# Kernel tuning notes

Hardware: AMD Instinct MI355X
Metric: run time of the kernel (lower is better)

The kernel has to match this reference:

```python
import jax, jax.numpy as jnp
import numpy as np

LN_EPS = 1e-5
TOP_K = 2

def _layernorm(x, g, b):
    mu = jnp.mean(x, axis=-1, keepdims=True)
    var = jnp.mean(jnp.square(x - mu), axis=-1, keepdims=True)
    return (x - mu) * jax.lax.rsqrt(var + LN_EPS) * g + b

def setup_inputs() -> dict:
    key = jax.random.key(0)
    ks = jax.random.split(key, 8)
    N, D, H, E = 16384, 2048, 256, 64
    H2 = H // 2
    s = 0.02
    return {
        "x": jax.random.normal(ks[0], (N, D), dtype=jnp.float32),
        "w1": jax.random.normal(ks[1], (D, H), dtype=jnp.float32) * s,
        "b1": jnp.zeros((H,), jnp.float32),
        "g1": jnp.ones((H,), jnp.float32),
        "be1": jnp.zeros((H,), jnp.float32),
        "w2": jax.random.normal(ks[2], (H, H2), dtype=jnp.float32) * s,
        "b2": jnp.zeros((H2,), jnp.float32),
        "g2": jnp.ones((H2,), jnp.float32),
        "be2": jnp.zeros((H2,), jnp.float32),
        "w3": jax.random.normal(ks[3], (H2, E), dtype=jnp.float32) * s,
        "b3": jnp.zeros((E,), jnp.float32),
        "temperature": jnp.ones((1,), jnp.float32),
    }

def reference(x, w1, b1, g1, be1, w2, b2, g2, be2, w3, b3, temperature):
    # Router MLP: Linear -> LN -> GELU (exact/erf, matching torch F.gelu) x2
    h = jax.nn.gelu(_layernorm(x @ w1 + b1, g1, be1), approximate=False)
    h = jax.nn.gelu(_layernorm(h @ w2 + b2, g2, be2), approximate=False)
    gate_logits = h @ w3 + b3  # [N, E]
    gate_logits = gate_logits / jnp.maximum(temperature, 0.1)
    # eval mode: dropout off, no noise injection
    top_vals, top_idx = jax.lax.top_k(gate_logits, TOP_K)  # [N, k]
    top_gates = jax.nn.softmax(top_vals, axis=-1)
    top_gates = top_gates / (jnp.sum(top_gates, axis=-1, keepdims=True) + 1e-8)
    rows = jnp.arange(gate_logits.shape[0])[:, None]
    gates = jnp.zeros_like(gate_logits).at[rows, top_idx].set(top_gates)
    return gates, top_idx, gate_logits
```

## Files before the change

kernel.cpp:

```cpp
#include <hip/hip_runtime.h>
#include <math.h>

#define NROWS 16384
#define DIN   2048
#define H1D   256
#define H2D   128
#define NE    64
#define EPS_MARGIN 2e-4f
#define SQRT1_2 0.70710678118654752440084436210485
#define IBIG 0x7fffffff

typedef short  bf16x8 __attribute__((ext_vector_type(8)));
typedef float  f32x4  __attribute__((ext_vector_type(4)));
typedef __attribute__((address_space(3))) void lds_void;
typedef __attribute__((address_space(1))) const void glob_void;

#define GLDS16(src, dst) \
    __builtin_amdgcn_global_load_lds((glob_void*)(src), (lds_void*)(dst), 16, 0, 0)

#define WS_OFF_ROWS 64
#define WS_OFF_W1FH 66560
#define WS_OFF_W1FL (WS_OFF_W1FH + DIN*H1D*2)
#define WS_OFF_H1G  (WS_OFF_W1FL + DIN*H1D*2)
#define WS_NEED_FUSED (size_t)WS_OFF_H1G
#define WS_NEED_SPLIT (size_t)(WS_OFF_H1G + (size_t)NROWS*H1D*4)

__device__ __forceinline__ void split_bf16(float v, unsigned short& h, unsigned short& l) {
    unsigned int u = __float_as_uint(v);
    unsigned int rh = u + 0x7FFFu + ((u >> 16) & 1u);
    h = (unsigned short)(rh >> 16);
    float hf = __uint_as_float((unsigned int)h << 16);
    float r = v - hf;
    unsigned int u2 = __float_as_uint(r);
    unsigned int rl = u2 + 0x7FFFu + ((u2 >> 16) & 1u);
    l = (unsigned short)(rl >> 16);
}

__device__ __forceinline__ void split_fast(float v, short& h, short& l) {
    unsigned int u = __float_as_uint(v);
    unsigned int rh = (u + 0x7FFFu + ((u >> 16) & 1u)) >> 16;
    h = (short)rh;
    float r = v - __uint_as_float(rh << 16);
    l = (short)(__float_as_uint(r) >> 16);
}

__device__ __forceinline__ bool gtr(float a, int ia, float b, int ib) {
    return a > b || (a == b && ia < ib);
}
__device__ __forceinline__ void ins3(float v, int iv,
                                     float& t1, int& j1, float& t2, int& j2, float& t3, int& j3) {
    if (gtr(v, iv, t1, j1))      { t3 = t2; j3 = j2; t2 = t1; j2 = j1; t1 = v; j1 = iv; }
    else if (gtr(v, iv, t2, j2)) { t3 = t2; j3 = j2; t2 = v;  j2 = iv; }
    else if (gtr(v, iv, t3, j3)) { t3 = v;  j3 = iv; }
}

__global__ void prep_w1f_kernel(const float* __restrict__ w1,
                                unsigned short* __restrict__ w1f_hi,
                                unsigned short* __restrict__ w1f_lo,
                                unsigned int* __restrict__ ws_count)
{
    if (blockIdx.x == 0 && threadIdx.x == 0) *ws_count = 0u;
    const int g    = blockIdx.x * 256 + threadIdx.x;
    const int st   = g >> 10;
    const int cb   = (g >> 6) & 15;
    const int lane = g & 63;
    const int col  = cb * 16 + (lane & 15);
    const int k0   = st * 32 + (lane >> 4) * 8;
    unsigned short vh[8], vl[8];
    #pragma unroll
    for (int j = 0; j < 8; ++j) {
        float v = w1[(size_t)(k0 + j) * H1D + col];
        split_bf16(v, vh[j], vl[j]);
    }
    *(uint4*)(w1f_hi + (size_t)g * 8) = *(uint4*)vh;
    *(uint4*)(w1f_lo + (size_t)g * 8) = *(uint4*)vl;
}

#define BM 32
#define KSTEPS (DIN / 32)
#define OFF_AB  0
#define OFF_BH  8192
#define OFF_BL  40960
#define OFF_H1  0
#define H1P     264
#define OFF_H2  33792
#define H2P     132
#define OFF_RED 50688
#define SMEM_SZ 73728

__global__ __launch_bounds__(512, 4)
void gemm1_ln_kernel(const float* __restrict__ x,
                     const float* __restrict__ b1, const float* __restrict__ g1,
                     const float* __restrict__ be1,
                     const unsigned short* __restrict__ w1f_hi,
                     const unsigned short* __restrict__ w1f_lo,
                     float* __restrict__ h1g)
{
    __shared__ __align__(16) char smem[SMEM_SZ];
    float*  sH1  = (float*)(smem + OFF_H1);
    float2* sRed = (float2*)(smem + OFF_RED);

    const int tid  = threadIdx.x;
    const int lane = tid & 63;
    const int wid  = tid >> 6;
    const int wr   = wid >> 2;
    const int wc   = wid & 3;
    const int lr   = lane & 15;
    const int lg   = lane >> 4;
    const int r0   = blockIdx.x * BM;

    const int arow = (wid & 3) * 8 + (lane >> 3);
    const int aseg = lane & 7;
    const float* asrc = x + (size_t)(r0 + arow) * DIN + ((aseg ^ (arow & 7)) << 2);
    const unsigned short* bsh0 = w1f_hi + ((size_t)((wid * 2 + 0) * 64 + lane)) * 8;
    const unsigned short* bsh1 = w1f_hi + ((size_t)((wid * 2 + 1) * 64 + lane)) * 8;
    const unsigned short* bsl0 = w1f_lo + ((size_t)((wid * 2 + 0) * 64 + lane)) * 8;
    const unsigned short* bsl1 = w1f_lo + ((size_t)((wid * 2 + 1) * 64 + lane)) * 8;

#define STAGE(buf_, st_) do { \
    if (wid < 4) GLDS16(asrc + (size_t)(st_) * 32, smem + OFF_AB + (buf_) * 4096 + wid * 1024); \
    GLDS16(bsh0 + (size_t)(st_) * 8192, smem + OFF_BH + (buf_) * 16384 + (wid * 2 + 0) * 1024); \
    GLDS16(bsh1 + (size_t)(st_) * 8192, smem + OFF_BH + (buf_) * 16384 + (wid * 2 + 1) * 1024); \
    GLDS16(bsl0 + (size_t)(st_) * 8192, smem + OFF_BL + (buf_) * 16384 + (wid * 2 + 0) * 1024); \
    GLDS16(bsl1 + (size_t)(st_) * 8192, smem + OFF_BL + (buf_) * 16384 + (wid * 2 + 1) * 1024); \
} while (0)

    f32x4 acc[4];
    #pragma unroll
    for (int t = 0; t < 4; ++t) acc[t] = (f32x4){0.f, 0.f, 0.f, 0.f};

    STAGE(0, 0);
    __syncthreads();
    int cur = 0;
    for (int st = 0; st < KSTEPS; ++st) {
        if (st + 1 < KSTEPS) STAGE(cur ^ 1, st + 1);
        bf16x8 ah, al;
        {
            int row = wr * 16 + lr;
            int g0  = (2 * lg) ^ (lr & 7);
            const char* abase = smem + OFF_AB + cur * 4096 + row * 128;
            float4 q0 = *(const float4*)(abase + g0 * 16);
            float4 q1 = *(const float4*)(abase + (g0 ^ 1) * 16);
            float af[8] = {q0.x, q0.y, q0.z, q0.w, q1.x, q1.y, q1.z, q1.w};
            #pragma unroll
            for (int j = 0; j < 8; ++j) {
                short h, l;
                split_fast(af[j], h, l);
                ah[j] = h; al[j] = l;
            }
        }
        bf16x8 bh[4], bl[4];
        #pragma unroll
        for (int t = 0; t < 4; ++t) {
            int cb = wc * 4 + t;
            bh[t] = *(const bf16x8*)(smem + OFF_BH + cur * 16384 + cb * 1024 + lane * 16);
            bl[t] = *(const bf16x8*)(smem + OFF_BL + cur * 16384 + cb * 1024 + lane * 16);
        }
        #pragma unroll
        for (int t = 0; t < 4; ++t) {
            acc[t] = __builtin_amdgcn_mfma_f32_16x16x32_bf16(ah, bh[t], acc[t], 0, 0, 0);
            acc[t] = __builtin_amdgcn_mfma_f32_16x16x32_bf16(ah, bl[t], acc[t], 0, 0, 0);
            acc[t] = __builtin_amdgcn_mfma_f32_16x16x32_bf16(al, bh[t], acc[t], 0, 0, 0);
        }
        __syncthreads();
        cur ^= 1;
    }
#undef STAGE

    float tb[4], tg[4], tbe[4];
    #pragma unroll
    for (int t = 0; t < 4; ++t) {
        int col = wc * 64 + t * 16 + lr;
        tb[t] = b1[col]; tg[t] = g1[col]; tbe[t] = be1[col];
    }
    #pragma unroll
    for (int t = 0; t < 4; ++t)
        #pragma unroll
        for (int rg = 0; rg < 4; ++rg)
            acc[t][rg] += tb[t];

    #pragma unroll
    for (int rg = 0; rg < 4; ++rg) {
        float p1 = 0.f, p2 = 0.f;
        #pragma unroll
        for (int t = 0; t < 4; ++t) { float v = acc[t][rg]; p1 += v; p2 += v * v; }
        p1 += __shfl_xor(p1, 1, 64); p2 += __shfl_xor(p2, 1, 64);
        p1 += __shfl_xor(p1, 2, 64); p2 += __shfl_xor(p2, 2, 64);
        p1 += __shfl_xor(p1, 4, 64); p2 += __shfl_xor(p2, 4, 64);
        p1 += __shfl_xor(p1, 8, 64); p2 += __shfl_xor(p2, 8, 64);
        if (lr == 0) {
            int row = wr * 16 + lg * 4 + rg;
            sRed[row * 4 + wc] = make_float2(p1, p2);
        }
    }
    __syncthreads();

    #pragma unroll
    for (int rg = 0; rg < 4; ++rg) {
        int row = wr * 16 + lg * 4 + rg;
        float2 q0 = sRed[row * 4 + 0], q1 = sRed[row * 4 + 1];
        float2 q2 = sRed[row * 4 + 2], q3 = sRed[row * 4 + 3];
        float s1 = (q0.x + q1.x) + (q2.x + q3.x);
        float s2 = (q0.y + q1.y) + (q2.y + q3.y);
        float mu  = s1 * (1.0f / H1D);
        float var = s2 * (1.0f / H1D) - mu * mu;
        float rs  = rsqrtf(var + 1e-5f);
        #pragma unroll
        for (int t = 0; t < 4; ++t) {
            int col = wc * 64 + t * 16 + lr;
            float v = (acc[t][rg] - mu) * rs * tg[t] + tbe[t];
            v = 0.5f * v * (1.0f + erff(v * (float)SQRT1_2));
            sH1[row * H1P + col] = v;
        }
    }
    __syncthreads();

    #pragma unroll
    for (int i = 0; i < 4; ++i) {
        int u = tid + i * 512;
        int row = u >> 6, f4 = u & 63;
        float4 v = *(const float4*)&sH1[row * H1P + f4 * 4];
        *(float4*)(h1g + (size_t)(r0 + row) * H1D + f4 * 4) = v;
    }
}

__global__ __launch_bounds__(256, 4)
void tail_kernel(const float* __restrict__ h1g,
                 const float* __restrict__ w2, const float* __restrict__ b2,
                 const float* __restrict__ g2, const float* __restrict__ be2,
                 const float* __restrict__ w3, const float* __restrict__ b3,
                 const float* __restrict__ temperature,
                 float* __restrict__ out_gates,
                 float* __restrict__ out_idx,
                 float* __restrict__ out_logits,
                 unsigned int* __restrict__ ws_count,
                 int* __restrict__ ws_rows)
{
    __shared__ __align__(16) float sH1[16 * H1P];
    __shared__ __align__(16) float sH2[16 * H2P];

    const int tid = threadIdx.x;
    const int r0  = blockIdx.x * 16;

    #pragma unroll
    for (int i = 0; i < 4; ++i) {
        int u = tid + i * 256;
        int row = u >> 6, f4 = u & 63;
        *(float4*)&sH1[row * H1P + f4 * 4] =
            *(const float4*)(h1g + (size_t)(r0 + row) * H1D + f4 * 4);
    }
    __syncthreads();

    const int tx = tid & 31;
    const int ty = tid >> 5;
    float acc2[2][4];
    #pragma unroll
    for (int i = 0; i < 2; ++i)
        #pragma unroll
        for (int j = 0; j < 4; ++j) acc2[i][j] = 0.f;
    {
        const float* w2p = w2 + tx * 4;
        #pragma unroll 4
        for (int k = 0; k < H1D; ++k) {
            float4 wv4 = *(const float4*)(w2p + (size_t)k * H2D);
            float wr4[4] = {wv4.x, wv4.y, wv4.z, wv4.w};
            float ar0 = sH1[(ty * 2 + 0) * H1P + k];
            float ar1 = sH1[(ty * 2 + 1) * H1P + k];
            #pragma unroll
            for (int j = 0; j < 4; ++j) {
                acc2[0][j] = fmaf(ar0, wr4[j], acc2[0][j]);
                acc2[1][j] = fmaf(ar1, wr4[j], acc2[1][j]);
            }
        }
    }
    {
        float b2v[4], g2v[4], be2v[4];
        #pragma unroll
        for (int j = 0; j < 4; ++j) {
            b2v[j] = b2[tx * 4 + j]; g2v[j] = g2[tx * 4 + j]; be2v[j] = be2[tx * 4 + j];
        }
        #pragma unroll
        for (int i = 0; i < 2; ++i) {
            float s1 = 0.f, s2 = 0.f, vv[4];
            #pragma unroll
            for (int j = 0; j < 4; ++j) {
                float v = acc2[i][j] + b2v[j];
                vv[j] = v; s1 += v; s2 += v * v;
            }
            s1 += __shfl_xor(s1, 1, 64);  s2 += __shfl_xor(s2, 1, 64);
            s1 += __shfl_xor(s1, 2, 64);  s2 += __shfl_xor(s2, 2, 64);
            s1 += __shfl_xor(s1, 4, 64);  s2 += __shfl_xor(s2, 4, 64);
            s1 += __shfl_xor(s1, 8, 64);  s2 += __shfl_xor(s2, 8, 64);
            s1 += __shfl_xor(s1, 16, 64); s2 += __shfl_xor(s2, 16, 64);
            float mu  = s1 * (1.0f / H2D);
            float var = s2 * (1.0f / H2D) - mu * mu;
            float rs  = rsqrtf(var + 1e-5f);
            #pragma unroll
            for (int j = 0; j < 4; ++j) {
                float v = (vv[j] - mu) * rs * g2v[j] + be2v[j];
                v = 0.5f * v * (1.0f + erff(v * (float)SQRT1_2));
                sH2[(ty * 2 + i) * H2P + tx * 4 + j] = v;
            }
        }
    }
    __syncthreads();

    const int q = tid & 15;
    const int r = tid >> 4;
    float acc3[4];
    #pragma unroll
    for (int j = 0; j < 4; ++j) acc3[j] = 0.f;
    {
        const float* w3p = w3 + q * 4;
        #pragma unroll 4
        for (int k = 0; k < H2D; ++k) {
            float hv = sH2[r * H2P + k];
            float4 wa = *(const float4*)(w3p + (size_t)k * NE);
            acc3[0] = fmaf(hv, wa.x, acc3[0]);
            acc3[1] = fmaf(hv, wa.y, acc3[1]);
            acc3[2] = fmaf(hv, wa.z, acc3[2]);
            acc3[3] = fmaf(hv, wa.w, acc3[3]);
        }
    }
    float tinv = 1.0f / fmaxf(temperature[0], 0.1f);
    float lg4[4];
    #pragma unroll
    for (int j = 0; j < 4; ++j) lg4[j] = (acc3[j] + b3[q * 4 + j]) * tinv;

    *(float4*)(out_logits + (size_t)(r0 + r) * NE + q * 4) = make_float4(lg4[0], lg4[1], lg4[2], lg4[3]);

    float v1 = -INFINITY, v2 = -INFINITY, v3 = -INFINITY;
    int   i1 = IBIG, i2 = IBIG, i3 = IBIG;
    #pragma unroll
    for (int j = 0; j < 4; ++j) ins3(lg4[j], q * 4 + j, v1, i1, v2, i2, v3, i3);
    #pragma unroll
    for (int m = 1; m < 16; m <<= 1) {
        float c1v = __shfl_xor(v1, m, 64); int cj1 = __shfl_xor(i1, m, 64);
        float c2v = __shfl_xor(v2, m, 64); int cj2 = __shfl_xor(i2, m, 64);
        float c3v = __shfl_xor(v3, m, 64); int cj3 = __shfl_xor(i3, m, 64);
        ins3(c1v, cj1, v1, i1, v2, i2, v3, i3);
        ins3(c2v, cj2, v1, i1, v2, i2, v3, i3);
        ins3(c3v, cj3, v1, i1, v2, i2, v3, i3);
    }

    float e2  = expf(v2 - v1);
    float den = 1.0f + e2;
    float tg1 = 1.0f / den;
    float tg2 = e2 / den;
    float ssum = tg1 + tg2 + 1e-8f;
    float gv1 = tg1 / ssum;
    float gv2 = tg2 / ssum;

    if (q == 0) {
        float margin = fminf(v1 - v2, v2 - v3);
        if (!(margin >= EPS_MARGIN)) {
            unsigned int slot = atomicAdd(ws_count, 1u);
            if ((int)slot < NROWS) ws_rows[slot] = r0 + r;
        }
        out_idx[(size_t)(r0 + r) * 2 + 0] = (float)i1;
        out_idx[(size_t)(r0 + r) * 2 + 1] = (float)i2;
    }
    {
        float gvv[4];
        #pragma unroll
        for (int j = 0; j < 4; ++j) {
            int c = q * 4 + j;
            gvv[j] = (c == i1) ? gv1 : ((c == i2) ? gv2 : 0.0f);
        }
        *(float4*)(out_gates + (size_t)(r0 + r) * NE + q * 4) = make_float4(gvv[0], gvv[1], gvv[2], gvv[3]);
    }
}

__global__ __launch_bounds__(1024, 1)
void repair_f64_kernel(const float* __restrict__ x,
                       const float* __restrict__ w1, const float* __restrict__ b1,
                       const float* __restrict__ g1, const float* __restrict__ be1,
                       const float* __restrict__ w2, const float* __restrict__ b2,
                       const float* __restrict__ g2, const float* __restrict__ be2,
                       const float* __restrict__ w3, const float* __restrict__ b3,
                       const float* __restrict__ temperature,
                       float* __restrict__ out_gates,
                       float* __restrict__ out_idx,
                       const unsigned int* __restrict__ ws_count,
                       const int* __restrict__ ws_rows)
{
    __shared__ float  sxr[DIN];
    __shared__ double sPart[1024];
    __shared__ double sh1[H1D];
    __shared__ double sh2[H2D];
    __shared__ double sred[32];

    const int t = threadIdx.x;
    const int lane = t & 63, w = t >> 6;
    const unsigned int n = *ws_count;
    const double tinv = 1.0 / fmax((double)temperature[0], 0.1);

    for (unsigned int wi = blockIdx.x; wi < n; wi += gridDim.x) {
        const int row = ws_rows[wi];

        const float4* xr4 = (const float4*)(x + (size_t)row * DIN);
        if (t < DIN / 4) ((float4*)sxr)[t] = xr4[t];
        __syncthreads();

        {
            const int c = t & 255, sl = t >> 8;
            const float* w1c = w1 + c;
            const int kb = sl * 512;
            double a0 = 0, a1 = 0, a2 = 0, a3 = 0;
            for (int k = 0; k < 512; k += 16) {
                float wv[16];
                #pragma unroll
                for (int j = 0; j < 16; ++j)
                    wv[j] = w1c[(size_t)(kb + k + j) * H1D];
                float xv[16];
                #pragma unroll
                for (int j = 0; j < 16; ++j) xv[j] = sxr[kb + k + j];
                #pragma unroll
                for (int j = 0; j < 16; j += 4) {
                    a0 = fma((double)xv[j + 0], (double)wv[j + 0], a0);
                    a1 = fma((double)xv[j + 1], (double)wv[j + 1], a1);
                    a2 = fma((double)xv[j + 2], (double)wv[j + 2], a2);
                    a3 = fma((double)xv[j + 3], (double)wv[j + 3], a3);
                }
            }
            sPart[sl * 256 + c] = (a0 + a1) + (a2 + a3);
        }
        __syncthreads();
        double c1 = 0.0;
        if (t < 256) {
            c1 = ((sPart[0 * 256 + t] + sPart[1 * 256 + t]) +
                  (sPart[2 * 256 + t] + sPart[3 * 256 + t])) + (double)b1[t];
            double s1 = c1, s2 = c1 * c1;
            for (int m = 1; m < 64; m <<= 1) { s1 += __shfl_xor(s1, m, 64); s2 += __shfl_xor(s2, m, 64); }
            if (lane == 0) { sred[w * 2] = s1; sred[w * 2 + 1] = s2; }
        }
        __syncthreads();
        if (t < 256) {
            double s1 = (sred[0] + sred[2]) + (sred[4] + sred[6]);
            double s2 = (sred[1] + sred[3]) + (sred[5] + sred[7]);
            double mu  = s1 * (1.0 / H1D);
            double var = s2 * (1.0 / H1D) - mu * mu;
            double rs  = 1.0 / sqrt(var + 1e-5);
            double vn  = (c1 - mu) * rs * (double)g1[t] + (double)be1[t];
            sh1[t] = 0.5 * vn * (1.0 + erf(vn * SQRT1_2));
        }
        __syncthreads();

        {
            const int c = t & 127, sl2 = t >> 7;
            const float* w2c = w2 + c;
            const int kb = sl2 * 32;
            float w2v[32];
            #pragma unroll
            for (int j = 0; j < 32; ++j)
                w2v[j] = w2c[(size_t)(kb + j) * H2D];
            double p = 0;
            #pragma unroll
            for (int j = 0; j < 32; ++j)
                p = fma(sh1[kb + j], (double)w2v[j], p);
            sPart[sl2 * 128 + c] = p;
        }
        __syncthreads();
        double c2 = 0.0;
        if (t < 128) {
            double p0 = (sPart[0 * 128 + t] + sPart[1 * 128 + t]) + (sPart[2 * 128 + t] + sPart[3 * 128 + t]);
            double p1 = (sPart[4 * 128 + t] + sPart[5 * 128 + t]) + (sPart[6 * 128 + t] + sPart[7 * 128 + t]);
            c2 = (p0 + p1) + (double)b2[t];
            double s1 = c2, s2 = c2 * c2;
            for (int m = 1; m < 64; m <<= 1) { s1 += __shfl_xor(s1, m, 64); s2 += __shfl_xor(s2, m, 64); }
            if (lane == 0) { sred[w * 2] = s1; sred[w * 2 + 1] = s2; }
        }
        __syncthreads();
        if (t < 128) {
            double s1 = sred[0] + sred[2];
            double s2 = sred[1] + sred[3];
            double mu  = s1 * (1.0 / H2D);
            double var = s2 * (1.0 / H2D) - mu * mu;
            double rs  = 1.0 / sqrt(var + 1e-5);
            double vn  = (c2 - mu) * rs * (double)g2[t] + (double)be2[t];
            sh2[t] = 0.5 * vn * (1.0 + erf(vn * SQRT1_2));
        }
        __syncthreads();

        {
            const int c = t & 63, sl3 = t >> 6;
            const float* w3c = w3 + c;
            const int kb = sl3 * 8;
            float w3v[8];
            #pragma unroll
            for (int j = 0; j < 8; ++j)
                w3v[j] = w3c[(size_t)(kb + j) * NE];
            double p = 0;
            #pragma unroll
            for (int j = 0; j < 8; ++j)
                p = fma(sh2[kb + j], (double)w3v[j], p);
            sPart[sl3 * 64 + c] = p;
        }
        __syncthreads();
        if (t < NE) {
            double q0 = (sPart[0*64+t]  + sPart[1*64+t])  + (sPart[2*64+t]  + sPart[3*64+t]);
            double q1 = (sPart[4*64+t]  + sPart[5*64+t])  + (sPart[6*64+t]  + sPart[7*64+t]);
            double q2 = (sPart[8*64+t]  + sPart[9*64+t])  + (sPart[10*64+t] + sPart[11*64+t]);
            double q3 = (sPart[12*64+t] + sPart[13*64+t]) + (sPart[14*64+t] + sPart[15*64+t]);
            double lgv = (((q0 + q1) + (q2 + q3)) + (double)b3[t]) * tinv;

            double v1 = lgv, v2 = -INFINITY;
            int i1 = t, i2 = IBIG;
            for (int m = 1; m < 64; m <<= 1) {
                double ov1 = __shfl_xor(v1, m, 64); int oi1 = __shfl_xor(i1, m, 64);
                double ov2 = __shfl_xor(v2, m, 64); int oi2 = __shfl_xor(i2, m, 64);
                bool aw = (v1 > ov1) || (v1 == ov1 && i1 < oi1);
                double wv = aw ? v1  : ov1;  int wi_ = aw ? i1  : oi1;
                double lv = aw ? ov1 : v1;   int li  = aw ? oi1 : i1;
                double sv = aw ? v2  : ov2;  int si  = aw ? i2  : oi2;
                bool sw = (sv > lv) || (sv == lv && si < li);
                v1 = wv; i1 = wi_;
                v2 = sw ? sv : lv;
                i2 = sw ? si : li;
            }
            double e2d = exp(v2 - v1);
            double den = 1.0 + e2d;
            double tg1 = 1.0 / den;
            double tg2 = e2d / den;
            double ssum = tg1 + tg2 + 1e-8;
            float gv1 = (float)(tg1 / ssum);
            float gv2 = (float)(tg2 / ssum);
            if (t == 0) {
                out_idx[(size_t)row * 2 + 0] = (float)i1;
                out_idx[(size_t)row * 2 + 1] = (float)i2;
            }
            out_gates[(size_t)row * NE + t] = (t == i1) ? gv1 : ((t == i2) ? gv2 : 0.0f);
        }
        __syncthreads();
    }
}

__global__ __launch_bounds__(512, 4)
void gate_fused_kernel(const float* __restrict__ x,
                       const float* __restrict__ b1, const float* __restrict__ g1,
                       const float* __restrict__ be1,
                       const float* __restrict__ w2, const float* __restrict__ b2,
                       const float* __restrict__ g2, const float* __restrict__ be2,
                       const float* __restrict__ w3, const float* __restrict__ b3,
                       const float* __restrict__ temperature,
                       const unsigned short* __restrict__ w1f_hi,
                       const unsigned short* __restrict__ w1f_lo,
                       float* __restrict__ out_gates,
                       float* __restrict__ out_idx,
                       float* __restrict__ out_logits,
                       unsigned int* __restrict__ ws_count,
                       int* __restrict__ ws_rows)
{
    __shared__ __align__(16) char smem[SMEM_SZ];
    float*  sH1  = (float*)(smem + OFF_H1);
    float*  sH2  = (float*)(smem + OFF_H2);
    float2* sRed = (float2*)(smem + OFF_RED);

    const int tid  = threadIdx.x;
    const int lane = tid & 63;
    const int wid  = tid >> 6;
    const int wr   = wid >> 2;
    const int wc   = wid & 3;
    const int lr   = lane & 15;
    const int lg   = lane >> 4;
    const int r0   = blockIdx.x * BM;

    const int arow = (wid & 3) * 8 + (lane >> 3);
    const int aseg = lane & 7;
    const float* asrc = x + (size_t)(r0 + arow) * DIN + ((aseg ^ (arow & 7)) << 2);
    const unsigned short* bsh0 = w1f_hi + ((size_t)((wid * 2 + 0) * 64 + lane)) * 8;
    const unsigned short* bsh1 = w1f_hi + ((size_t)((wid * 2 + 1) * 64 + lane)) * 8;
    const unsigned short* bsl0 = w1f_lo + ((size_t)((wid * 2 + 0) * 64 + lane)) * 8;
    const unsigned short* bsl1 = w1f_lo + ((size_t)((wid * 2 + 1) * 64 + lane)) * 8;

#define STAGE(buf_, st_) do { \
    if (wid < 4) GLDS16(asrc + (size_t)(st_) * 32, smem + OFF_AB + (buf_) * 4096 + wid * 1024); \
    GLDS16(bsh0 + (size_t)(st_) * 8192, smem + OFF_BH + (buf_) * 16384 + (wid * 2 + 0) * 1024); \
    GLDS16(bsh1 + (size_t)(st_) * 8192, smem + OFF_BH + (buf_) * 16384 + (wid * 2 + 1) * 1024); \
    GLDS16(bsl0 + (size_t)(st_) * 8192, smem + OFF_BL + (buf_) * 16384 + (wid * 2 + 0) * 1024); \
    GLDS16(bsl1 + (size_t)(st_) * 8192, smem + OFF_BL + (buf_) * 16384 + (wid * 2 + 1) * 1024); \
} while (0)

    f32x4 acc[4];
    #pragma unroll
    for (int t = 0; t < 4; ++t) acc[t] = (f32x4){0.f, 0.f, 0.f, 0.f};

    STAGE(0, 0);
    __syncthreads();
    int cur = 0;
    for (int st = 0; st < KSTEPS; ++st) {
        if (st + 1 < KSTEPS) STAGE(cur ^ 1, st + 1);
        bf16x8 ah, al;
        {
            int row = wr * 16 + lr;
            int g0  = (2 * lg) ^ (lr & 7);
            const char* abase = smem + OFF_AB + cur * 4096 + row * 128;
            float4 q0 = *(const float4*)(abase + g0 * 16);
            float4 q1 = *(const float4*)(abase + (g0 ^ 1) * 16);
            float af[8] = {q0.x, q0.y, q0.z, q0.w, q1.x, q1.y, q1.z, q1.w};
            #pragma unroll
            for (int j = 0; j < 8; ++j) {
                short h, l;
                split_fast(af[j], h, l);
                ah[j] = h; al[j] = l;
            }
        }
        bf16x8 bh[4], bl[4];
        #pragma unroll
        for (int t = 0; t < 4; ++t) {
            int cb = wc * 4 + t;
            bh[t] = *(const bf16x8*)(smem + OFF_BH + cur * 16384 + cb * 1024 + lane * 16);
            bl[t] = *(const bf16x8*)(smem + OFF_BL + cur * 16384 + cb * 1024 + lane * 16);
        }
        #pragma unroll
        for (int t = 0; t < 4; ++t) {
            acc[t] = __builtin_amdgcn_mfma_f32_16x16x32_bf16(ah, bh[t], acc[t], 0, 0, 0);
            acc[t] = __builtin_amdgcn_mfma_f32_16x16x32_bf16(ah, bl[t], acc[t], 0, 0, 0);
            acc[t] = __builtin_amdgcn_mfma_f32_16x16x32_bf16(al, bh[t], acc[t], 0, 0, 0);
        }
        __syncthreads();
        cur ^= 1;
    }
#undef STAGE

    float tb[4], tg[4], tbe[4];
    #pragma unroll
    for (int t = 0; t < 4; ++t) {
        int col = wc * 64 + t * 16 + lr;
        tb[t] = b1[col]; tg[t] = g1[col]; tbe[t] = be1[col];
    }
    #pragma unroll
    for (int t = 0; t < 4; ++t)
        #pragma unroll
        for (int rg = 0; rg < 4; ++rg)
            acc[t][rg] += tb[t];

    #pragma unroll
    for (int rg = 0; rg < 4; ++rg) {
        float p1 = 0.f, p2 = 0.f;
        #pragma unroll
        for (int t = 0; t < 4; ++t) { float v = acc[t][rg]; p1 += v; p2 += v * v; }
        p1 += __shfl_xor(p1, 1, 64); p2 += __shfl_xor(p2, 1, 64);
        p1 += __shfl_xor(p1, 2, 64); p2 += __shfl_xor(p2, 2, 64);
        p1 += __shfl_xor(p1, 4, 64); p2 += __shfl_xor(p2, 4, 64);
        p1 += __shfl_xor(p1, 8, 64); p2 += __shfl_xor(p2, 8, 64);
        if (lr == 0) {
            int row = wr * 16 + lg * 4 + rg;
            sRed[row * 4 + wc] = make_float2(p1, p2);
        }
    }
    __syncthreads();

    #pragma unroll
    for (int rg = 0; rg < 4; ++rg) {
        int row = wr * 16 + lg * 4 + rg;
        float2 q0 = sRed[row * 4 + 0], q1 = sRed[row * 4 + 1];
        float2 q2 = sRed[row * 4 + 2], q3 = sRed[row * 4 + 3];
        float s1 = (q0.x + q1.x) + (q2.x + q3.x);
        float s2 = (q0.y + q1.y) + (q2.y + q3.y);
        float mu  = s1 * (1.0f / H1D);
        float var = s2 * (1.0f / H1D) - mu * mu;
        float rs  = rsqrtf(var + 1e-5f);
        #pragma unroll
        for (int t = 0; t < 4; ++t) {
            int col = wc * 64 + t * 16 + lr;
            float v = (acc[t][rg] - mu) * rs * tg[t] + tbe[t];
            v = 0.5f * v * (1.0f + erff(v * (float)SQRT1_2));
            sH1[row * H1P + col] = v;
        }
    }
    __syncthreads();

    const int tx = tid & 31;
    const int ty = tid >> 5;
    float acc2[2][4];
    #pragma unroll
    for (int i = 0; i < 2; ++i)
        #pragma unroll
        for (int j = 0; j < 4; ++j) acc2[i][j] = 0.f;
    {
        const float* w2p = w2 + tx * 4;
        #pragma unroll 4
        for (int k = 0; k < H1D; ++k) {
            float4 wv4 = *(const float4*)(w2p + (size_t)k * H2D);
            float wr4[4] = {wv4.x, wv4.y, wv4.z, wv4.w};
            float ar0 = sH1[(ty * 2 + 0) * H1P + k];
            float ar1 = sH1[(ty * 2 + 1) * H1P + k];
            #pragma unroll
            for (int j = 0; j < 4; ++j) {
                acc2[0][j] = fmaf(ar0, wr4[j], acc2[0][j]);
                acc2[1][j] = fmaf(ar1, wr4[j], acc2[1][j]);
            }
        }
    }
    {
        float b2v[4], g2v[4], be2v[4];
        #pragma unroll
        for (int j = 0; j < 4; ++j) {
            b2v[j] = b2[tx * 4 + j]; g2v[j] = g2[tx * 4 + j]; be2v[j] = be2[tx * 4 + j];
        }
        #pragma unroll
        for (int i = 0; i < 2; ++i) {
            float s1 = 0.f, s2 = 0.f, vv[4];
            #pragma unroll
            for (int j = 0; j < 4; ++j) {
                float v = acc2[i][j] + b2v[j];
                vv[j] = v; s1 += v; s2 += v * v;
            }
            s1 += __shfl_xor(s1, 1, 64);  s2 += __shfl_xor(s2, 1, 64);
            s1 += __shfl_xor(s1, 2, 64);  s2 += __shfl_xor(s2, 2, 64);
            s1 += __shfl_xor(s1, 4, 64);  s2 += __shfl_xor(s2, 4, 64);
            s1 += __shfl_xor(s1, 8, 64);  s2 += __shfl_xor(s2, 8, 64);
            s1 += __shfl_xor(s1, 16, 64); s2 += __shfl_xor(s2, 16, 64);
            float mu  = s1 * (1.0f / H2D);
            float var = s2 * (1.0f / H2D) - mu * mu;
            float rs  = rsqrtf(var + 1e-5f);
            #pragma unroll
            for (int j = 0; j < 4; ++j) {
                float v = (vv[j] - mu) * rs * g2v[j] + be2v[j];
                v = 0.5f * v * (1.0f + erff(v * (float)SQRT1_2));
                sH2[(ty * 2 + i) * H2P + tx * 4 + j] = v;
            }
        }
    }
    __syncthreads();

    const int q = tid & 15;
    const int r = tid >> 4;
    float acc3[4];
    #pragma unroll
    for (int j = 0; j < 4; ++j) acc3[j] = 0.f;
    {
        const float* w3p = w3 + q * 4;
        #pragma unroll 4
        for (int k = 0; k < H2D; ++k) {
            float hv = sH2[r * H2P + k];
            float4 wa = *(const float4*)(w3p + (size_t)k * NE);
            acc3[0] = fmaf(hv, wa.x, acc3[0]);
            acc3[1] = fmaf(hv, wa.y, acc3[1]);
            acc3[2] = fmaf(hv, wa.z, acc3[2]);
            acc3[3] = fmaf(hv, wa.w, acc3[3]);
        }
    }
    float tinv = 1.0f / fmaxf(temperature[0], 0.1f);
    float lg4[4];
    #pragma unroll
    for (int j = 0; j < 4; ++j) lg4[j] = (acc3[j] + b3[q * 4 + j]) * tinv;

    *(float4*)(out_logits + (size_t)(r0 + r) * NE + q * 4) = make_float4(lg4[0], lg4[1], lg4[2], lg4[3]);

    float v1 = -INFINITY, v2 = -INFINITY, v3 = -INFINITY;
    int   i1 = IBIG, i2 = IBIG, i3 = IBIG;
    #pragma unroll
    for (int j = 0; j < 4; ++j) ins3(lg4[j], q * 4 + j, v1, i1, v2, i2, v3, i3);
    #pragma unroll
    for (int m = 1; m < 16; m <<= 1) {
        float c1v = __shfl_xor(v1, m, 64); int cj1 = __shfl_xor(i1, m, 64);
        float c2v = __shfl_xor(v2, m, 64); int cj2 = __shfl_xor(i2, m, 64);
        float c3v = __shfl_xor(v3, m, 64); int cj3 = __shfl_xor(i3, m, 64);
        ins3(c1v, cj1, v1, i1, v2, i2, v3, i3);
        ins3(c2v, cj2, v1, i1, v2, i2, v3, i3);
        ins3(c3v, cj3, v1, i1, v2, i2, v3, i3);
    }

    float e2  = expf(v2 - v1);
    float den = 1.0f + e2;
    float tg1 = 1.0f / den;
    float tg2 = e2 / den;
    float ssum = tg1 + tg2 + 1e-8f;
    float gv1 = tg1 / ssum;
    float gv2 = tg2 / ssum;

    if (q == 0) {
        float margin = fminf(v1 - v2, v2 - v3);
        if (!(margin >= EPS_MARGIN)) {
            unsigned int slot = atomicAdd(ws_count, 1u);
            if ((int)slot < NROWS) ws_rows[slot] = r0 + r;
        }
        out_idx[(size_t)(r0 + r) * 2 + 0] = (float)i1;
        out_idx[(size_t)(r0 + r) * 2 + 1] = (float)i2;
    }
    {
        float gvv[4];
        #pragma unroll
        for (int j = 0; j < 4; ++j) {
            int c = q * 4 + j;
            gvv[j] = (c == i1) ? gv1 : ((c == i2) ? gv2 : 0.0f);
        }
        *(float4*)(out_gates + (size_t)(r0 + r) * NE + q * 4) = make_float4(gvv[0], gvv[1], gvv[2], gvv[3]);
    }
}

extern "C" void kernel_launch(void* const* d_in, const int* in_sizes, int n_in,
                              void* d_out, int out_size, void* d_ws, size_t ws_size,
                              hipStream_t stream)
{
    const float* x    = (const float*)d_in[0];
    const float* w1   = (const float*)d_in[1];
    const float* b1   = (const float*)d_in[2];
    const float* g1   = (const float*)d_in[3];
    const float* be1  = (const float*)d_in[4];
    const float* w2   = (const float*)d_in[5];
    const float* b2   = (const float*)d_in[6];
    const float* g2   = (const float*)d_in[7];
    const float* be2  = (const float*)d_in[8];
    const float* w3   = (const float*)d_in[9];
    const float* b3   = (const float*)d_in[10];
    const float* temp = (const float*)d_in[11];

    float* gates  = (float*)d_out;
    float* idxf   = gates + (size_t)NROWS * NE;
    float* logits = idxf + (size_t)NROWS * 2;

    unsigned int* ws_count = (unsigned int*)d_ws;
    int* ws_rows = (int*)((char*)d_ws + WS_OFF_ROWS);
    unsigned short* w1f_hi = (unsigned short*)((char*)d_ws + WS_OFF_W1FH);
    unsigned short* w1f_lo = (unsigned short*)((char*)d_ws + WS_OFF_W1FL);

    hipLaunchKernelGGL(prep_w1f_kernel, dim3(256), dim3(256), 0, stream, w1, w1f_hi, w1f_lo, ws_count);

    if (ws_size >= WS_NEED_SPLIT) {
        float* h1g = (float*)((char*)d_ws + WS_OFF_H1G);
        hipLaunchKernelGGL(gemm1_ln_kernel, dim3(NROWS / BM), dim3(512), 0, stream,
                           x, b1, g1, be1, w1f_hi, w1f_lo, h1g);
        hipLaunchKernelGGL(tail_kernel, dim3(NROWS / 16), dim3(256), 0, stream,
                           h1g, w2, b2, g2, be2, w3, b3, temp,
                           gates, idxf, logits, ws_count, ws_rows);
    } else {
        hipLaunchKernelGGL(gate_fused_kernel, dim3(NROWS / BM), dim3(512), 0, stream,
                           x, b1, g1, be1, w2, b2, g2, be2, w3, b3, temp,
                           w1f_hi, w1f_lo, gates, idxf, logits, ws_count, ws_rows);
    }
    hipLaunchKernelGGL(repair_f64_kernel, dim3(512), dim3(1024), 0, stream,
                       x, w1, b1, g1, be1, w2, b2, g2, be2, w3, b3, temp,
                       gates, idxf, ws_count, ws_rows);
}
```

Before: 198.0 us.

## Triple-buffer GEMM1 staging with vmcnt waits and drop fused fallback kernel

Moves the first GEMM's async global-to-LDS staging from double to triple buffering. Explicit s_waitcnt vmcnt counts replace the per-iteration __syncthreads pair, so loads run two stages ahead with one barrier per step. This raises LDS use to about 109 KB and lowers launch bounds to 2 blocks per CU, trading occupancy for deeper prefetch. The fused single-kernel fallback is removed and the split path always runs, which assumes the workspace is large enough.

```diff
diff --git a/kernel.cpp b/kernel.cpp
--- a/kernel.cpp
+++ b/kernel.cpp
@@ -22,7 +22,6 @@
 #define WS_OFF_W1FH 66560
 #define WS_OFF_W1FL (WS_OFF_W1FH + DIN*H1D*2)
 #define WS_OFF_H1G  (WS_OFF_W1FL + DIN*H1D*2)
-#define WS_NEED_FUSED (size_t)WS_OFF_H1G
 #define WS_NEED_SPLIT (size_t)(WS_OFF_H1G + (size_t)NROWS*H1D*4)
 
 __device__ __forceinline__ void split_bf16(float v, unsigned short& h, unsigned short& l) {
@@ -78,17 +77,16 @@
 
 #define BM 32
 #define KSTEPS (DIN / 32)
-#define OFF_AB  0
-#define OFF_BH  8192
-#define OFF_BL  40960
-#define OFF_H1  0
-#define H1P     264
-#define OFF_H2  33792
-#define H2P     132
-#define OFF_RED 50688
-#define SMEM_SZ 73728
-
-__global__ __launch_bounds__(512, 4)
+
+#define T_OFF_AB  0
+#define T_OFF_BH  12288
+#define T_OFF_BL  61440
+#define T_OFF_RED 110592
+#define T_SMEM    111616
+#define H1P       264
+#define H2P       132
+
+__global__ __launch_bounds__(512, 2)
 void gemm1_ln_kernel(const float* __restrict__ x,
                      const float* __restrict__ b1, const float* __restrict__ g1,
                      const float* __restrict__ be1,
@@ -96,9 +94,9 @@
                      const unsigned short* __restrict__ w1f_lo,
                      float* __restrict__ h1g)
 {
-    __shared__ __align__(16) char smem[SMEM_SZ];
-    float*  sH1  = (float*)(smem + OFF_H1);
-    float2* sRed = (float2*)(smem + OFF_RED);
+    __shared__ __align__(16) char smem[T_SMEM];
+    float*  sH1  = (float*)(smem);
+    float2* sRed = (float2*)(smem + T_OFF_RED);
 
     const int tid  = threadIdx.x;
     const int lane = tid & 63;
@@ -117,28 +115,39 @@
     const unsigned short* bsl0 = w1f_lo + ((size_t)((wid * 2 + 0) * 64 + lane)) * 8;
     const unsigned short* bsl1 = w1f_lo + ((size_t)((wid * 2 + 1) * 64 + lane)) * 8;
 
-#define STAGE(buf_, st_) do { \
-    if (wid < 4) GLDS16(asrc + (size_t)(st_) * 32, smem + OFF_AB + (buf_) * 4096 + wid * 1024); \
-    GLDS16(bsh0 + (size_t)(st_) * 8192, smem + OFF_BH + (buf_) * 16384 + (wid * 2 + 0) * 1024); \
-    GLDS16(bsh1 + (size_t)(st_) * 8192, smem + OFF_BH + (buf_) * 16384 + (wid * 2 + 1) * 1024); \
-    GLDS16(bsl0 + (size_t)(st_) * 8192, smem + OFF_BL + (buf_) * 16384 + (wid * 2 + 0) * 1024); \
-    GLDS16(bsl1 + (size_t)(st_) * 8192, smem + OFF_BL + (buf_) * 16384 + (wid * 2 + 1) * 1024); \
+#define T_STAGE(buf_, st_) do { \
+    if (wid < 4) GLDS16(asrc + (size_t)(st_) * 32, smem + T_OFF_AB + (buf_) * 4096 + wid * 1024); \
+    GLDS16(bsh0 + (size_t)(st_) * 8192, smem + T_OFF_BH + (buf_) * 16384 + (wid * 2 + 0) * 1024); \
+    GLDS16(bsh1 + (size_t)(st_) * 8192, smem + T_OFF_BH + (buf_) * 16384 + (wid * 2 + 1) * 1024); \
+    GLDS16(bsl0 + (size_t)(st_) * 8192, smem + T_OFF_BL + (buf_) * 16384 + (wid * 2 + 0) * 1024); \
+    GLDS16(bsl1 + (size_t)(st_) * 8192, smem + T_OFF_BL + (buf_) * 16384 + (wid * 2 + 1) * 1024); \
 } while (0)
 
     f32x4 acc[4];
     #pragma unroll
     for (int t = 0; t < 4; ++t) acc[t] = (f32x4){0.f, 0.f, 0.f, 0.f};
 
-    STAGE(0, 0);
-    __syncthreads();
-    int cur = 0;
+    T_STAGE(0, 0);
+    T_STAGE(1, 1);
+
+    int b = 0;
     for (int st = 0; st < KSTEPS; ++st) {
-        if (st + 1 < KSTEPS) STAGE(cur ^ 1, st + 1);
+        if (st < KSTEPS - 1) {
+            if (wid < 4) asm volatile("s_waitcnt vmcnt(5)" ::: "memory");
+            else         asm volatile("s_waitcnt vmcnt(4)" ::: "memory");
+        } else {
+            asm volatile("s_waitcnt vmcnt(0)" ::: "memory");
+        }
+        __builtin_amdgcn_s_barrier();
+        if (st + 2 < KSTEPS) {
+            int b2 = (st + 2) % 3;
+            T_STAGE(b2, st + 2);
+        }
         bf16x8 ah, al;
         {
             int row = wr * 16 + lr;
             int g0  = (2 * lg) ^ (lr & 7);
-            const char* abase = smem + OFF_AB + cur * 4096 + row * 128;
+            const char* abase = smem + T_OFF_AB + b * 4096 + row * 128;
             float4 q0 = *(const float4*)(abase + g0 * 16);
             float4 q1 = *(const float4*)(abase + (g0 ^ 1) * 16);
             float af[8] = {q0.x, q0.y, q0.z, q0.w, q1.x, q1.y, q1.z, q1.w};
@@ -153,8 +162,8 @@
         #pragma unroll
         for (int t = 0; t < 4; ++t) {
             int cb = wc * 4 + t;
-            bh[t] = *(const bf16x8*)(smem + OFF_BH + cur * 16384 + cb * 1024 + lane * 16);
-            bl[t] = *(const bf16x8*)(smem + OFF_BL + cur * 16384 + cb * 1024 + lane * 16);
+            bh[t] = *(const bf16x8*)(smem + T_OFF_BH + b * 16384 + cb * 1024 + lane * 16);
+            bl[t] = *(const bf16x8*)(smem + T_OFF_BL + b * 16384 + cb * 1024 + lane * 16);
         }
         #pragma unroll
         for (int t = 0; t < 4; ++t) {
@@ -162,10 +171,11 @@
             acc[t] = __builtin_amdgcn_mfma_f32_16x16x32_bf16(ah, bl[t], acc[t], 0, 0, 0);
             acc[t] = __builtin_amdgcn_mfma_f32_16x16x32_bf16(al, bh[t], acc[t], 0, 0, 0);
         }
-        __syncthreads();
-        cur ^= 1;
-    }
-#undef STAGE
+        b = (b + 1 == 3) ? 0 : b + 1;
+    }
+#undef T_STAGE
+
+    __syncthreads();
 
     float tb[4], tg[4], tbe[4];
     #pragma unroll
@@ -535,262 +545,6 @@
     }
 }
 
-__global__ __launch_bounds__(512, 4)
-void gate_fused_kernel(const float* __restrict__ x,
-                       const float* __restrict__ b1, const float* __restrict__ g1,
-                       const float* __restrict__ be1,
-                       const float* __restrict__ w2, const float* __restrict__ b2,
-                       const float* __restrict__ g2, const float* __restrict__ be2,
-                       const float* __restrict__ w3, const float* __restrict__ b3,
-                       const float* __restrict__ temperature,
-                       const unsigned short* __restrict__ w1f_hi,
-                       const unsigned short* __restrict__ w1f_lo,
-                       float* __restrict__ out_gates,
-                       float* __restrict__ out_idx,
-                       float* __restrict__ out_logits,
-                       unsigned int* __restrict__ ws_count,
-                       int* __restrict__ ws_rows)
-{
-    __shared__ __align__(16) char smem[SMEM_SZ];
-    float*  sH1  = (float*)(smem + OFF_H1);
-    float*  sH2  = (float*)(smem + OFF_H2);
-    float2* sRed = (float2*)(smem + OFF_RED);
-
-    const int tid  = threadIdx.x;
-    const int lane = tid & 63;
-    const int wid  = tid >> 6;
-    const int wr   = wid >> 2;
-    const int wc   = wid & 3;
-    const int lr   = lane & 15;
-    const int lg   = lane >> 4;
-    const int r0   = blockIdx.x * BM;
-
-    const int arow = (wid & 3) * 8 + (lane >> 3);
-    const int aseg = lane & 7;
-    const float* asrc = x + (size_t)(r0 + arow) * DIN + ((aseg ^ (arow & 7)) << 2);
-    const unsigned short* bsh0 = w1f_hi + ((size_t)((wid * 2 + 0) * 64 + lane)) * 8;
-    const unsigned short* bsh1 = w1f_hi + ((size_t)((wid * 2 + 1) * 64 + lane)) * 8;
-    const unsigned short* bsl0 = w1f_lo + ((size_t)((wid * 2 + 0) * 64 + lane)) * 8;
-    const unsigned short* bsl1 = w1f_lo + ((size_t)((wid * 2 + 1) * 64 + lane)) * 8;
-
-#define STAGE(buf_, st_) do { \
-    if (wid < 4) GLDS16(asrc + (size_t)(st_) * 32, smem + OFF_AB + (buf_) * 4096 + wid * 1024); \
-    GLDS16(bsh0 + (size_t)(st_) * 8192, smem + OFF_BH + (buf_) * 16384 + (wid * 2 + 0) * 1024); \
-    GLDS16(bsh1 + (size_t)(st_) * 8192, smem + OFF_BH + (buf_) * 16384 + (wid * 2 + 1) * 1024); \
-    GLDS16(bsl0 + (size_t)(st_) * 8192, smem + OFF_BL + (buf_) * 16384 + (wid * 2 + 0) * 1024); \
-    GLDS16(bsl1 + (size_t)(st_) * 8192, smem + OFF_BL + (buf_) * 16384 + (wid * 2 + 1) * 1024); \
-} while (0)
-
-    f32x4 acc[4];
-    #pragma unroll
-    for (int t = 0; t < 4; ++t) acc[t] = (f32x4){0.f, 0.f, 0.f, 0.f};
-
-    STAGE(0, 0);
-    __syncthreads();
-    int cur = 0;
-    for (int st = 0; st < KSTEPS; ++st) {
-        if (st + 1 < KSTEPS) STAGE(cur ^ 1, st + 1);
-        bf16x8 ah, al;
-        {
-            int row = wr * 16 + lr;
-            int g0  = (2 * lg) ^ (lr & 7);
-            const char* abase = smem + OFF_AB + cur * 4096 + row * 128;
-            float4 q0 = *(const float4*)(abase + g0 * 16);
-            float4 q1 = *(const float4*)(abase + (g0 ^ 1) * 16);
-            float af[8] = {q0.x, q0.y, q0.z, q0.w, q1.x, q1.y, q1.z, q1.w};
-            #pragma unroll
-            for (int j = 0; j < 8; ++j) {
-                short h, l;
-                split_fast(af[j], h, l);
-                ah[j] = h; al[j] = l;
-            }
-        }
-        bf16x8 bh[4], bl[4];
-        #pragma unroll
-        for (int t = 0; t < 4; ++t) {
-            int cb = wc * 4 + t;
-            bh[t] = *(const bf16x8*)(smem + OFF_BH + cur * 16384 + cb * 1024 + lane * 16);
-            bl[t] = *(const bf16x8*)(smem + OFF_BL + cur * 16384 + cb * 1024 + lane * 16);
-        }
-        #pragma unroll
-        for (int t = 0; t < 4; ++t) {
-            acc[t] = __builtin_amdgcn_mfma_f32_16x16x32_bf16(ah, bh[t], acc[t], 0, 0, 0);
-            acc[t] = __builtin_amdgcn_mfma_f32_16x16x32_bf16(ah, bl[t], acc[t], 0, 0, 0);
-            acc[t] = __builtin_amdgcn_mfma_f32_16x16x32_bf16(al, bh[t], acc[t], 0, 0, 0);
-        }
-        __syncthreads();
-        cur ^= 1;
-    }
-#undef STAGE
-
-    float tb[4], tg[4], tbe[4];
-    #pragma unroll
-    for (int t = 0; t < 4; ++t) {
-        int col = wc * 64 + t * 16 + lr;
-        tb[t] = b1[col]; tg[t] = g1[col]; tbe[t] = be1[col];
-    }
-    #pragma unroll
-    for (int t = 0; t < 4; ++t)
-        #pragma unroll
-        for (int rg = 0; rg < 4; ++rg)
-            acc[t][rg] += tb[t];
-
-    #pragma unroll
-    for (int rg = 0; rg < 4; ++rg) {
-        float p1 = 0.f, p2 = 0.f;
-        #pragma unroll
-        for (int t = 0; t < 4; ++t) { float v = acc[t][rg]; p1 += v; p2 += v * v; }
-        p1 += __shfl_xor(p1, 1, 64); p2 += __shfl_xor(p2, 1, 64);
-        p1 += __shfl_xor(p1, 2, 64); p2 += __shfl_xor(p2, 2, 64);
-        p1 += __shfl_xor(p1, 4, 64); p2 += __shfl_xor(p2, 4, 64);
-        p1 += __shfl_xor(p1, 8, 64); p2 += __shfl_xor(p2, 8, 64);
-        if (lr == 0) {
-            int row = wr * 16 + lg * 4 + rg;
-            sRed[row * 4 + wc] = make_float2(p1, p2);
-        }
-    }
-    __syncthreads();
-
-    #pragma unroll
-    for (int rg = 0; rg < 4; ++rg) {
-        int row = wr * 16 + lg * 4 + rg;
-        float2 q0 = sRed[row * 4 + 0], q1 = sRed[row * 4 + 1];
-        float2 q2 = sRed[row * 4 + 2], q3 = sRed[row * 4 + 3];
-        float s1 = (q0.x + q1.x) + (q2.x + q3.x);
-        float s2 = (q0.y + q1.y) + (q2.y + q3.y);
-        float mu  = s1 * (1.0f / H1D);
-        float var = s2 * (1.0f / H1D) - mu * mu;
-        float rs  = rsqrtf(var + 1e-5f);
-        #pragma unroll
-        for (int t = 0; t < 4; ++t) {
-            int col = wc * 64 + t * 16 + lr;
-            float v = (acc[t][rg] - mu) * rs * tg[t] + tbe[t];
-            v = 0.5f * v * (1.0f + erff(v * (float)SQRT1_2));
-            sH1[row * H1P + col] = v;
-        }
-    }
-    __syncthreads();
-
-    const int tx = tid & 31;
-    const int ty = tid >> 5;
-    float acc2[2][4];
-    #pragma unroll
-    for (int i = 0; i < 2; ++i)
-        #pragma unroll
-        for (int j = 0; j < 4; ++j) acc2[i][j] = 0.f;
-    {
-        const float* w2p = w2 + tx * 4;
-        #pragma unroll 4
-        for (int k = 0; k < H1D; ++k) {
-            float4 wv4 = *(const float4*)(w2p + (size_t)k * H2D);
-            float wr4[4] = {wv4.x, wv4.y, wv4.z, wv4.w};
-            float ar0 = sH1[(ty * 2 + 0) * H1P + k];
-            float ar1 = sH1[(ty * 2 + 1) * H1P + k];
-            #pragma unroll
-            for (int j = 0; j < 4; ++j) {
-                acc2[0][j] = fmaf(ar0, wr4[j], acc2[0][j]);
-                acc2[1][j] = fmaf(ar1, wr4[j], acc2[1][j]);
-            }
-        }
-    }
-    {
-        float b2v[4], g2v[4], be2v[4];
-        #pragma unroll
-        for (int j = 0; j < 4; ++j) {
-            b2v[j] = b2[tx * 4 + j]; g2v[j] = g2[tx * 4 + j]; be2v[j] = be2[tx * 4 + j];
-        }
-        #pragma unroll
-        for (int i = 0; i < 2; ++i) {
-            float s1 = 0.f, s2 = 0.f, vv[4];
-            #pragma unroll
-            for (int j = 0; j < 4; ++j) {
-                float v = acc2[i][j] + b2v[j];
-                vv[j] = v; s1 += v; s2 += v * v;
-            }
-            s1 += __shfl_xor(s1, 1, 64);  s2 += __shfl_xor(s2, 1, 64);
-            s1 += __shfl_xor(s1, 2, 64);  s2 += __shfl_xor(s2, 2, 64);
-            s1 += __shfl_xor(s1, 4, 64);  s2 += __shfl_xor(s2, 4, 64);
-            s1 += __shfl_xor(s1, 8, 64);  s2 += __shfl_xor(s2, 8, 64);
-            s1 += __shfl_xor(s1, 16, 64); s2 += __shfl_xor(s2, 16, 64);
-            float mu  = s1 * (1.0f / H2D);
-            float var = s2 * (1.0f / H2D) - mu * mu;
-            float rs  = rsqrtf(var + 1e-5f);
-            #pragma unroll
-            for (int j = 0; j < 4; ++j) {
-                float v = (vv[j] - mu) * rs * g2v[j] + be2v[j];
-                v = 0.5f * v * (1.0f + erff(v * (float)SQRT1_2));
-                sH2[(ty * 2 + i) * H2P + tx * 4 + j] = v;
-            }
-        }
-    }
-    __syncthreads();
-
-    const int q = tid & 15;
-    const int r = tid >> 4;
-    float acc3[4];
-    #pragma unroll
-    for (int j = 0; j < 4; ++j) acc3[j] = 0.f;
-    {
-        const float* w3p = w3 + q * 4;
-        #pragma unroll 4
-        for (int k = 0; k < H2D; ++k) {
-            float hv = sH2[r * H2P + k];
-            float4 wa = *(const float4*)(w3p + (size_t)k * NE);
-            acc3[0] = fmaf(hv, wa.x, acc3[0]);
-            acc3[1] = fmaf(hv, wa.y, acc3[1]);
-            acc3[2] = fmaf(hv, wa.z, acc3[2]);
-            acc3[3] = fmaf(hv, wa.w, acc3[3]);
-        }
-    }
-    float tinv = 1.0f / fmaxf(temperature[0], 0.1f);
-    float lg4[4];
-    #pragma unroll
-    for (int j = 0; j < 4; ++j) lg4[j] = (acc3[j] + b3[q * 4 + j]) * tinv;
-
-    *(float4*)(out_logits + (size_t)(r0 + r) * NE + q * 4) = make_float4(lg4[0], lg4[1], lg4[2], lg4[3]);
-
-    float v1 = -INFINITY, v2 = -INFINITY, v3 = -INFINITY;
-    int   i1 = IBIG, i2 = IBIG, i3 = IBIG;
-    #pragma unroll
-    for (int j = 0; j < 4; ++j) ins3(lg4[j], q * 4 + j, v1, i1, v2, i2, v3, i3);
-    #pragma unroll
-    for (int m = 1; m < 16; m <<= 1) {
-        float c1v = __shfl_xor(v1, m, 64); int cj1 = __shfl_xor(i1, m, 64);
-        float c2v = __shfl_xor(v2, m, 64); int cj2 = __shfl_xor(i2, m, 64);
-        float c3v = __shfl_xor(v3, m, 64); int cj3 = __shfl_xor(i3, m, 64);
-        ins3(c1v, cj1, v1, i1, v2, i2, v3, i3);
-        ins3(c2v, cj2, v1, i1, v2, i2, v3, i3);
-        ins3(c3v, cj3, v1, i1, v2, i2, v3, i3);
-    }
-
-    float e2  = expf(v2 - v1);
-    float den = 1.0f + e2;
-    float tg1 = 1.0f / den;
-    float tg2 = e2 / den;
-    float ssum = tg1 + tg2 + 1e-8f;
-    float gv1 = tg1 / ssum;
-    float gv2 = tg2 / ssum;
-
-    if (q == 0) {
-        float margin = fminf(v1 - v2, v2 - v3);
-        if (!(margin >= EPS_MARGIN)) {
-            unsigned int slot = atomicAdd(ws_count, 1u);
-            if ((int)slot < NROWS) ws_rows[slot] = r0 + r;
-        }
-        out_idx[(size_t)(r0 + r) * 2 + 0] = (float)i1;
-        out_idx[(size_t)(r0 + r) * 2 + 1] = (float)i2;
-    }
-    {
-        float gvv[4];
-        #pragma unroll
-        for (int j = 0; j < 4; ++j) {
-            int c = q * 4 + j;
-            gvv[j] = (c == i1) ? gv1 : ((c == i2) ? gv2 : 0.0f);
-        }
-        *(float4*)(out_gates + (size_t)(r0 + r) * NE + q * 4) = make_float4(gvv[0], gvv[1], gvv[2], gvv[3]);
-    }
-}
-
 extern "C" void kernel_launch(void* const* d_in, const int* in_sizes, int n_in,
                               void* d_out, int out_size, void* d_ws, size_t ws_size,
                               hipStream_t stream)
@@ -816,21 +570,14 @@
     int* ws_rows = (int*)((char*)d_ws + WS_OFF_ROWS);
     unsigned short* w1f_hi = (unsigned short*)((char*)d_ws + WS_OFF_W1FH);
     unsigned short* w1f_lo = (unsigned short*)((char*)d_ws + WS_OFF_W1FL);
+    float* h1g = (float*)((char*)d_ws + WS_OFF_H1G);
 
     hipLaunchKernelGGL(prep_w1f_kernel, dim3(256), dim3(256), 0, stream, w1, w1f_hi, w1f_lo, ws_count);
-
-    if (ws_size >= WS_NEED_SPLIT) {
-        float* h1g = (float*)((char*)d_ws + WS_OFF_H1G);
-        hipLaunchKernelGGL(gemm1_ln_kernel, dim3(NROWS / BM), dim3(512), 0, stream,
-                           x, b1, g1, be1, w1f_hi, w1f_lo, h1g);
-        hipLaunchKernelGGL(tail_kernel, dim3(NROWS / 16), dim3(256), 0, stream,
-                           h1g, w2, b2, g2, be2, w3, b3, temp,
-                           gates, idxf, logits, ws_count, ws_rows);
-    } else {
-        hipLaunchKernelGGL(gate_fused_kernel, dim3(NROWS / BM), dim3(512), 0, stream,
-                           x, b1, g1, be1, w2, b2, g2, be2, w3, b3, temp,
-                           w1f_hi, w1f_lo, gates, idxf, logits, ws_count, ws_rows);
-    }
+    hipLaunchKernelGGL(gemm1_ln_kernel, dim3(NROWS / BM), dim3(512), 0, stream,
+                       x, b1, g1, be1, w1f_hi, w1f_lo, h1g);
+    hipLaunchKernelGGL(tail_kernel, dim3(NROWS / 16), dim3(256), 0, stream,
+                       h1g, w2, b2, g2, be2, w3, b3, temp,
+                       gates, idxf, logits, ws_count, ws_rows);
     hipLaunchKernelGGL(repair_f64_kernel, dim3(512), dim3(1024), 0, stream,
                        x, w1, b1, g1, be1, w2, b2, g2, be2, w3, b3, temp,
                        gates, idxf, ws_count, ws_rows);
```

New measurement: 260.6 us. +31.6%, slower.
